# Performance work log

Measured on AMD Instinct MI355X. Metric: run time of the kernel, lower is better.

## Reference

```python
import jax, jax.numpy as jnp
import numpy as np

MAX_POSITION_INDEX = 100  # class attribute of PosEmbedding


def _build_pos_embed_table(embed_dim: int) -> jnp.ndarray:
    """Sinusoidal table of shape (MAX_POSITION_INDEX+1, embed_dim//2)."""
    half = embed_dim // 2
    X = jnp.arange(MAX_POSITION_INDEX + 1, dtype=jnp.float32)[:, None]
    X = X / jnp.power(10000.0, jnp.arange(0, half, 2, dtype=jnp.float32) / half)
    pe = jnp.zeros((MAX_POSITION_INDEX + 1, half), dtype=jnp.float32)
    pe = pe.at[:, 0::2].set(jnp.sin(X))
    pe = pe.at[:, 1::2].set(jnp.cos(X))
    return pe


def setup_inputs() -> dict:
    key = jax.random.key(0)
    k1, k2 = jax.random.split(key)
    B, S, E = 16, 8191, 768
    x = jax.random.normal(k1, (B, S + 1, E), dtype=jnp.float32)  # (B, S+1, E)
    pos = jax.random.randint(k2, (B, S, 3), 0, MAX_POSITION_INDEX + 1, dtype=jnp.int32)
    pos_embed = _build_pos_embed_table(E)  # (101, E//2), frozen buffer
    return {"x": x, "pos": pos, "pos_embed": pos_embed}


def reference(x, pos, pos_embed):
    # x: (B, S+1, E) float; pos: (B, S, 3) int; pos_embed: (101, E//2)
    B, S, _ = pos.shape
    E = x.shape[-1]
    dtype = x.dtype

    # --- positional embedding: two gathers concatenated along channels ---
    emb = jnp.concatenate(
        [pos_embed[pos[:, :, 1]], pos_embed[pos[:, :, 2]]], axis=-1
    ).astype(dtype)  # (B, S, E); embed_dim is even so no zero-pad column
    pos_embedding = jnp.concatenate(
        [jnp.zeros((B, 1, E), dtype), emb], axis=1
    )  # (B, S+1, E): zero row prepended (cls-token slot)

    # --- section embedding: strided one-hot via index arithmetic ---
    # Original loop: section_embedding[i, j+1, pos[i,j,0]::max_sections_i+1] = 1
    # Equivalent mask: k >= p  and  (k - p) % (max_sections_i + 1) == 0
    p = pos[:, :, 0]                       # (B, S) section index per token
    max_sec = jnp.max(p, axis=1)           # (B,) repeat_section_embedding=True
    stride = max_sec + 1                   # (B,)
    k = jnp.arange(E, dtype=pos.dtype)     # (E,)
    d = k[None, None, :] - p[:, :, None]   # (B, S, E)
    mask = (d >= 0) & (d % stride[:, None, None] == 0) & (max_sec[:, None, None] > 0)
    sec = mask.astype(dtype)               # (B, S, E)
    sec = jnp.concatenate([jnp.zeros((B, 1, E), dtype), sec], axis=1)  # (B, S+1, E)
    sec = jnp.flip(sec, axis=2)            # torch.flip(..., (2,))

    # learnable_weight=False -> plain sum; dropout_prob=0.0 -> identity
    return x + pos_embedding + sec
```

## Files before the change

### kernel.cpp

```cpp
#include <hip/hip_runtime.h>

#define NB 16
#define NS 8191
#define SP1 8192
#define NE 768
#define HALF 384
#define VPR (NE / 4)

__global__ __launch_bounds__(256) void maxsec_kernel(const int* __restrict__ pos,
                                                     int* __restrict__ maxsec) {
    int b = blockIdx.x;
    int t = threadIdx.x;
    const int* p = pos + (size_t)b * NS * 3;
    int m = 0;
    for (int s = t; s < NS; s += 256) {
        int v = p[s * 3];
        m = v > m ? v : m;
    }
    __shared__ int sm[256];
    sm[t] = m;
    __syncthreads();
    for (int off = 128; off > 0; off >>= 1) {
        if (t < off) {
            int o = sm[t + off];
            if (o > sm[t]) sm[t] = o;
        }
        __syncthreads();
    }
    if (t == 0) maxsec[b] = sm[0];
}

__global__ __launch_bounds__(192) void posembed_kernel(const float4* __restrict__ x,
                                                       const int* __restrict__ pos,
                                                       const float* __restrict__ pe,
                                                       const int* __restrict__ maxsec,
                                                       float4* __restrict__ out) {
    const int s = blockIdx.x;
    const int b = blockIdx.y;
    const int e4 = threadIdx.x;

    size_t idx = ((size_t)b * SP1 + s) * VPR + e4;
    float4 xv = x[idx];

    if (s == 0) {
        out[idx] = xv;
        return;
    }

    const int* pr = pos + ((size_t)b * NS + (s - 1)) * 3;
    int p0 = pr[0];
    int i1 = pr[1];
    int i2 = pr[2];
    int ms = maxsec[b];
    unsigned stride = (unsigned)(ms + 1);

    float4 o;
    float* op = (float*)&o;
    const float* xp = (const float*)&xv;

#pragma unroll
    for (int j = 0; j < 4; ++j) {
        int e = e4 * 4 + j;
        float emb = (e < HALF) ? pe[i1 * HALF + e] : pe[i2 * HALF + (e - HALF)];
        int d = (NE - 1 - e) - p0;
        float sec = 0.0f;
        if (ms > 0 && d >= 0 && ((unsigned)d % stride) == 0u) sec = 1.0f;
        op[j] = xp[j] + emb + sec;
    }
    out[idx] = o;
}

extern "C" void kernel_launch(void* const* d_in, const int* in_sizes, int n_in,
                              void* d_out, int out_size, void* d_ws, size_t ws_size,
                              hipStream_t stream) {
    const float* x   = (const float*)d_in[0];
    const int*   pos = (const int*)d_in[1];
    const float* pe  = (const float*)d_in[2];
    float* out = (float*)d_out;
    int* maxsec = (int*)d_ws;

    maxsec_kernel<<<NB, 256, 0, stream>>>(pos, maxsec);

    dim3 grid(SP1, NB);
    posembed_kernel<<<grid, 192, 0, stream>>>((const float4*)x, pos, pe, maxsec,
                                              (float4*)out);
}
```

Baseline: 172.4 us.

## Process four rows per block with nontemporal vector IO and magic-number modulo

Each block now handles four sequence rows, batching the x loads up front so more memory requests are in flight. Loads and stores of the x and out streams use nontemporal hints. The table gather becomes a single float4 load, and the per-element modulo is replaced by a precomputed reciprocal multiply plus a decrementing counter. This targets a bandwidth-bound streaming kernel but uses more registers per thread and launches fewer blocks.

```diff
diff --git a/kernel.cpp b/kernel.cpp
--- a/kernel.cpp
+++ b/kernel.cpp
@@ -6,9 +6,13 @@
 #define NE 768
 #define HALF 384
 #define VPR (NE / 4)
+#define RPB 4
+
+typedef float f32x4 __attribute__((ext_vector_type(4)));
 
 __global__ __launch_bounds__(256) void maxsec_kernel(const int* __restrict__ pos,
-                                                     int* __restrict__ maxsec) {
+                                                     int* __restrict__ maxsec,
+                                                     unsigned* __restrict__ magics) {
     int b = blockIdx.x;
     int t = threadIdx.x;
     const int* p = pos + (size_t)b * NS * 3;
@@ -27,47 +31,66 @@
         }
         __syncthreads();
     }
-    if (t == 0) maxsec[b] = sm[0];
+    if (t == 0) {
+        int ms = sm[0];
+        maxsec[b] = ms;
+        unsigned stride = (unsigned)(ms + 1);
+        magics[b] = (0x100000u + stride - 1u) / stride;
+    }
 }
 
-__global__ __launch_bounds__(192) void posembed_kernel(const float4* __restrict__ x,
+__global__ __launch_bounds__(192) void posembed_kernel(const f32x4* __restrict__ x,
                                                        const int* __restrict__ pos,
-                                                       const float* __restrict__ pe,
+                                                       const f32x4* __restrict__ pe4,
                                                        const int* __restrict__ maxsec,
-                                                       float4* __restrict__ out) {
-    const int s = blockIdx.x;
+                                                       const unsigned* __restrict__ magics,
+                                                       f32x4* __restrict__ out) {
     const int b = blockIdx.y;
-    const int e4 = threadIdx.x;
+    const int s0 = blockIdx.x * RPB;
+    const int t = threadIdx.x;
 
-    size_t idx = ((size_t)b * SP1 + s) * VPR + e4;
-    float4 xv = x[idx];
+    const int ms = maxsec[b];
+    const unsigned stride = (unsigned)(ms + 1);
+    const unsigned magic = magics[b];
 
-    if (s == 0) {
-        out[idx] = xv;
-        return;
-    }
+    const size_t base = ((size_t)b * SP1 + s0) * VPR + t;
 
-    const int* pr = pos + ((size_t)b * NS + (s - 1)) * 3;
-    int p0 = pr[0];
-    int i1 = pr[1];
-    int i2 = pr[2];
-    int ms = maxsec[b];
-    unsigned stride = (unsigned)(ms + 1);
-
-    float4 o;
-    float* op = (float*)&o;
-    const float* xp = (const float*)&xv;
+    f32x4 xv[RPB];
+#pragma unroll
+    for (int r = 0; r < RPB; ++r)
+        xv[r] = __builtin_nontemporal_load(&x[base + (size_t)r * VPR]);
 
 #pragma unroll
-    for (int j = 0; j < 4; ++j) {
-        int e = e4 * 4 + j;
-        float emb = (e < HALF) ? pe[i1 * HALF + e] : pe[i2 * HALF + (e - HALF)];
-        int d = (NE - 1 - e) - p0;
-        float sec = 0.0f;
-        if (ms > 0 && d >= 0 && ((unsigned)d % stride) == 0u) sec = 1.0f;
-        op[j] = xp[j] + emb + sec;
+    for (int r = 0; r < RPB; ++r) {
+        const int s = s0 + r;
+        f32x4 o;
+        if (s == 0) {
+            o = xv[r];
+        } else {
+            const int* pr = pos + ((size_t)b * NS + (s - 1)) * 3;
+            const int p0 = pr[0];
+            const int i1 = pr[1];
+            const int i2 = pr[2];
+
+            f32x4 emb = (t < HALF / 4) ? pe4[i1 * (HALF / 4) + t]
+                                       : pe4[i2 * (HALF / 4) + (t - HALF / 4)];
+
+            f32x4 secs = {0.f, 0.f, 0.f, 0.f};
+            const int d0 = (NE - 1) - 4 * t - p0;
+            if (ms > 0 && d0 >= 0) {
+                unsigned ud = (unsigned)d0;
+                unsigned m = ud - stride * ((ud * magic) >> 20);
+#pragma unroll
+                for (int j = 0; j < 4; ++j) {
+                    if (d0 - j >= 0 && m == 0u) secs[j] = 1.0f;
+                    m = (m == 0u) ? stride - 1u : m - 1u;
+                }
+            }
+
+            o = xv[r] + emb + secs;
+        }
+        __builtin_nontemporal_store(o, &out[base + (size_t)r * VPR]);
     }
-    out[idx] = o;
 }
 
 extern "C" void kernel_launch(void* const* d_in, const int* in_sizes, int n_in,
@@ -78,10 +101,12 @@
     const float* pe  = (const float*)d_in[2];
     float* out = (float*)d_out;
     int* maxsec = (int*)d_ws;
+    unsigned* magics = (unsigned*)((char*)d_ws + NB * sizeof(int));
 
-    maxsec_kernel<<<NB, 256, 0, stream>>>(pos, maxsec);
+    maxsec_kernel<<<NB, 256, 0, stream>>>(pos, maxsec, magics);
 
-    dim3 grid(SP1, NB);
-    posembed_kernel<<<grid, 192, 0, stream>>>((const float4*)x, pos, pe, maxsec,
-                                              (float4*)out);
+    dim3 grid(SP1 / RPB, NB);
+    posembed_kernel<<<grid, 192, 0, stream>>>((const f32x4*)x, pos,
+                                              (const f32x4*)pe, maxsec, magics,
+                                              (f32x4*)out);
 }
```

Result: faster. 145.1 us (-15.8%).
